# Kernel tuning notes

Measured on AMD Instinct MI355X. Metric: run time of the kernel, lower is better.

The kernel has to match this reference:

```python
import jax, jax.numpy as jnp
import numpy as np
import math

B, NTOK, NH, D = 8, 1000, 8, 64
CHUNK = 8  # query-chunk size for the pairwise L1 score computation


def _linearm(w, x):
    # LinearM: w [out, in+1] (last column is bias); x [b, t, in] -> [b, t, out]
    return jnp.einsum('oi,bti->bto', w[:, :-1], x) + w[:, -1]


def setup_inputs() -> dict:
    key = jax.random.key(0)
    ks = jax.random.split(key, 4)
    scl = 0.005
    x = jax.random.normal(ks[0], (B, NTOK, D), dtype=jnp.float32)
    wq = (scl * jax.random.normal(ks[1], (NH * D, D + 1), dtype=jnp.float32)).at[:, -1].set(0.0)
    wv = (scl * jax.random.normal(ks[2], (NH * D, D + 1), dtype=jnp.float32)).at[:, -1].set(0.0)
    wk = scl * jnp.ones((NH, D), dtype=jnp.float32)
    wf = (scl * jax.random.normal(ks[3], (D, D + 1), dtype=jnp.float32)).at[:, -1].set(0.0)
    return {"x": x, "wq": wq, "wv": wv, "wk": wk, "wf": wf}


def _forward(x, wq, wv, wk, wf):
    b, t, d = x.shape
    nh = wk.shape[0]
    scale = 1.0 / math.sqrt(d)

    q = _linearm(wq, x).reshape(b, t, nh, d)          # [b, t, nh, d]
    v = _linearm(wv, x).reshape(b, t, nh, d)          # [b, t, nh, d]
    k = x[:, :, None, :] * wk[None, None]             # [b, t, nh, d]

    # L1-distance attention scores: a[b, s, q, h] = -scale * sum_w |q[b,q,h,w] - k[b,s,h,w]|
    # Computed in query chunks so the [b, t, t, nh, d] pairwise tensor is never materialized.
    nc = t // CHUNK
    qc = q.reshape(b, nc, CHUNK, nh, d).transpose(1, 0, 2, 3, 4)  # [nc, b, C, nh, d]

    @jax.checkpoint
    def scores(qch):
        # qch: [b, C, nh, d] -> [b, t(src), C, nh]
        return -scale * jnp.sum(jnp.abs(qch[:, None] - k[:, :, None]), axis=-1)

    a = jax.lax.map(scores, qc)                       # [nc, b, t, C, nh]
    a = a.transpose(1, 2, 0, 3, 4).reshape(b, t, t, nh)  # [b, src, dst, nh]

    # Extra all-zero "null" source row (mirrors a[:, a2len, :, :] = 0 before softmax)
    a = jnp.concatenate([a, jnp.zeros((b, 1, t, nh), a.dtype)], axis=1)
    a = jax.nn.softmax(a, axis=1)[:, :t]              # softmax over sources, drop null row

    # einsum('bsdh,bshw->bdhw') followed by sum over heads, fused:
    out = jnp.einsum('bsth,bshw->btw', a, v)          # [b, t, d]

    y = jax.nn.relu(out)                              # self.gelu is actually ReLU
    y = _linearm(wf, y)
    return x + y


def reference(x, wq, wv, wk, wf):
    return _forward(x, wq, wv, wk, wf)
```

## Files before the change

### kernel.cpp

```cpp
#include <hip/hip_runtime.h>
#include <math.h>

#define Bb 8
#define Tt 1000
#define TPAD 1024
#define NHh 8
#define Dd 64

typedef short bf16x8 __attribute__((ext_vector_type(8)));
typedef float f32x4 __attribute__((ext_vector_type(4)));

#define QOFF (-0.3f)
#define QSTEP (0.6f / 256.0f)
#define QINV (256.0f / 0.6f)
#define CQ (-0.125f * 1.44269504088896341f * QSTEP)

__device__ __forceinline__ unsigned sad_u8(unsigned a, unsigned b, unsigned c) {
#if __has_builtin(__builtin_amdgcn_sad_u8)
    return __builtin_amdgcn_sad_u8(a, b, c);
#else
    unsigned d;
    asm("v_sad_u8 %0, %1, %2, %3" : "=v"(d) : "v"(a), "v"(b), "v"(c));
    return d;
#endif
}

__device__ __forceinline__ unsigned quant8(float v) {
    float t = (v - QOFF) * QINV + 0.5f;
    t = fminf(fmaxf(t, 0.0f), 255.0f);
    return (unsigned)(int)t;
}

__device__ __forceinline__ unsigned cvt_pk_bf16(float lo, float hi) {
    unsigned r;
    asm("v_cvt_pk_bf16_f32 %0, %1, %2" : "=v"(r) : "v"(lo), "v"(hi));
    return r;
}

__device__ __forceinline__ bf16x8 mkbf(unsigned u0, unsigned u1, unsigned u2, unsigned u3) {
    union { unsigned u[4]; bf16x8 v; } x;
    x.u[0] = u0; x.u[1] = u1; x.u[2] = u2; x.u[3] = u3;
    return x.v;
}

__device__ __forceinline__ bf16x8 bfc(uint4 q) {
    union { uint4 q; bf16x8 v; } x; x.q = q; return x.v;
}

#define GLDS(gsrc, ldst) \
    __builtin_amdgcn_global_load_lds((const __attribute__((address_space(1))) unsigned*)(gsrc), \
                                     (__attribute__((address_space(3))) unsigned*)(ldst), 16, 0, 0)

__global__ __launch_bounds__(256) void prep_kernel(
    const float* __restrict__ x, const float* __restrict__ wq,
    const float* __restrict__ wv, const float* __restrict__ wk,
    unsigned* __restrict__ qq8, unsigned* __restrict__ kq8,
    uint4* __restrict__ vfrag)
{
    __shared__ float xs[64][68];
    __shared__ float ws[64][65];
    __shared__ float vS[64][68];
    const int tid = threadIdx.x;
    const int st = blockIdx.x;
    const int cb = blockIdx.y;
    const int b  = blockIdx.z;
    const bool isQ = (cb < 8);
    const int h = isQ ? cb : (cb - 8);
    const float* W = isQ ? wq : wv;
    const int cBase = h * 64;
    const int bh = b * NHh + h;

#pragma unroll
    for (int i = 0; i < 4; ++i) {
        int f4 = tid + i * 256;
        int r = f4 >> 4, c4 = (f4 & 15) << 2;
        int row = st * 64 + r; if (row >= Tt) row = Tt - 1;
        *(float4*)&xs[r][c4] = *(const float4*)&x[((size_t)b * Tt + row) * 64 + c4];
    }
#pragma unroll
    for (int i = 0; i < 16; ++i) {
        int idx = tid + i * 256;
        int c = idx >> 6, k = idx & 63;
        ws[c][k] = W[(cBase + c) * 65 + k];
    }
    __syncthreads();

    const int rg = tid >> 4, cg = tid & 15;
    const int r0 = rg * 4, c0 = cg * 4;
    float acc[4][4];
#pragma unroll
    for (int j = 0; j < 4; ++j) {
        float bias = W[(cBase + c0 + j) * 65 + 64];
#pragma unroll
        for (int i = 0; i < 4; ++i) acc[i][j] = bias;
    }
    for (int k0 = 0; k0 < 64; k0 += 4) {
        float4 a[4];
#pragma unroll
        for (int i = 0; i < 4; ++i) a[i] = *(const float4*)&xs[r0 + i][k0];
#pragma unroll
        for (int j = 0; j < 4; ++j) {
            float b0 = ws[c0 + j][k0 + 0];
            float b1 = ws[c0 + j][k0 + 1];
            float b2 = ws[c0 + j][k0 + 2];
            float b3 = ws[c0 + j][k0 + 3];
#pragma unroll
            for (int i = 0; i < 4; ++i)
                acc[i][j] += a[i].x * b0 + a[i].y * b1 + a[i].z * b2 + a[i].w * b3;
        }
    }

    if (isQ) {
#pragma unroll
        for (int i = 0; i < 4; ++i) {
            int t = st * 64 + r0 + i;
            unsigned d = 0u;
            if (t < Tt)
                d = quant8(acc[i][0]) | (quant8(acc[i][1]) << 8) |
                    (quant8(acc[i][2]) << 16) | (quant8(acc[i][3]) << 24);
            qq8[((size_t)bh * TPAD + t) * 16 + cg] = d;
        }
        {
            const int r = tid >> 2, c4 = tid & 3;
            const int t = st * 64 + r;
            unsigned kd[4];
            if (t < Tt) {
#pragma unroll
                for (int dw = 0; dw < 4; ++dw) {
                    int w = c4 * 16 + dw * 4;
                    float4 wkv = *(const float4*)&wk[h * 64 + w];
                    kd[dw] = quant8(xs[r][w + 0] * wkv.x) |
                             (quant8(xs[r][w + 1] * wkv.y) << 8) |
                             (quant8(xs[r][w + 2] * wkv.z) << 16) |
                             (quant8(xs[r][w + 3] * wkv.w) << 24);
                }
            } else {
                kd[0] = kd[1] = kd[2] = kd[3] = 0u;
            }
            const int c4s = c4 ^ ((r >> 3) & 3);
            *(uint4*)&kq8[((size_t)bh * TPAD + t) * 16 + c4s * 4] =
                make_uint4(kd[0], kd[1], kd[2], kd[3]);
        }
    } else {
#pragma unroll
        for (int i = 0; i < 4; ++i) {
            float4 o; o.x = acc[i][0]; o.y = acc[i][1]; o.z = acc[i][2]; o.w = acc[i][3];
            *(float4*)&vS[r0 + i][c0] = o;
        }
        __syncthreads();
#pragma unroll
        for (int e2 = 0; e2 < 2; ++e2) {
            int ent = tid + e2 * 256;
            int kk = ent >> 8, rem = ent & 255, n = rem >> 6, lane = rem & 63;
            int ts = kk * 32 + ((lane >> 4) << 3);
            int w  = n * 16 + (lane & 15);
            unsigned o[4];
#pragma unroll
            for (int pr = 0; pr < 4; ++pr) {
                int t0 = st * 64 + ts + pr * 2;
                float lo = (t0 < Tt)     ? vS[ts + pr * 2][w]     : 0.0f;
                float hi = (t0 + 1 < Tt) ? vS[ts + pr * 2 + 1][w] : 0.0f;
                o[pr] = cvt_pk_bf16(lo, hi);
            }
            vfrag[(((size_t)bh * 16 + st) * 8 + (kk * 4 + n)) * 64 + lane] =
                make_uint4(o[0], o[1], o[2], o[3]);
        }
    }
}

__global__ __launch_bounds__(256) void attn_kernel(
    const unsigned* __restrict__ qq8, const unsigned* __restrict__ kq8,
    const uint4* __restrict__ vfrag, float* __restrict__ part)
{
    __shared__ uint4 smem[1024];
    __shared__ float dred[2][2][16];

    const int tid = threadIdx.x;
    const int wv_ = tid >> 6;
    const int l   = tid & 63;
    const int g   = l >> 4;
    const int m   = l & 15;
    const int qt  = blockIdx.x;
    const int h   = blockIdx.y, b = blockIdx.z;
    const int bh  = b * NHh + h;
    const int rowhalf  = wv_ & 1;
    const int tilehalf = wv_ >> 1;
    const int rowbase  = qt * 64 + rowhalf * 32;

    unsigned qa[16], qb[16];
    {
        const uint4* qp = (const uint4*)qq8 + ((size_t)bh * TPAD + rowbase + m) * 4;
        *(uint4*)&qa[0]  = qp[0];  *(uint4*)&qa[4]  = qp[1];
        *(uint4*)&qa[8]  = qp[2];  *(uint4*)&qa[12] = qp[3];
        const uint4* qp2 = qp + 64;
        *(uint4*)&qb[0]  = qp2[0]; *(uint4*)&qb[4]  = qp2[1];
        *(uint4*)&qb[8]  = qp2[2]; *(uint4*)&qb[12] = qp2[3];
    }

    const uint4* kg = (const uint4*)kq8 + (size_t)bh * 4096;
    const uint4* vg = vfrag + (size_t)bh * 8192;

#define STAGEK(I, BUF) do { \
        GLDS(kg + (I) * 256 + wv_ * 64 + l,       &smem[(0 * 2 + (BUF)) * 256 + wv_ * 64]); \
        GLDS(kg + (8 + (I)) * 256 + wv_ * 64 + l, &smem[(1 * 2 + (BUF)) * 256 + wv_ * 64]); \
    } while (0)

    STAGEK(0, 0);
    __syncthreads();

    f32x4 aca[4], acb[4];
#pragma unroll
    for (int n = 0; n < 4; ++n) { aca[n] = (f32x4){0.f,0.f,0.f,0.f}; acb[n] = aca[n]; }
    float dsum_a = 0.0f, dsum_b = 0.0f;

#pragma unroll 1
    for (int i = 0; i < 8; ++i) {
        const int cur = i & 1;
        const int t = tilehalf * 8 + i;
        const uint4* kbase = &smem[(tilehalf * 2 + cur) * 256];
        const uint4* vt = vg + (size_t)t * 512 + l;

        if (i < 7) STAGEK(i + 1, cur ^ 1);

        uint4 vf0 = vt[0 * 64], vf1 = vt[1 * 64], vf2 = vt[2 * 64], vf3 = vt[3 * 64];

        bf16x8 Aa0, Ab0;
        {
            float pa[8], pb[8];
#pragma unroll
            for (int e = 0; e < 8; ++e) {
                const uint4* kb = kbase + ((g << 3) + e) * 4;
                uint4 c0 = kb[0 ^ g], c1 = kb[1 ^ g], c2 = kb[2 ^ g], c3 = kb[3 ^ g];
                const unsigned* k0 = (const unsigned*)&c0;
                const unsigned* k1 = (const unsigned*)&c1;
                const unsigned* k2 = (const unsigned*)&c2;
                const unsigned* k3 = (const unsigned*)&c3;
                unsigned sa0 = 0u, sa1 = 0u, sb0 = 0u, sb1 = 0u;
#pragma unroll
                for (int w = 0; w < 4; ++w) {
                    sa0 = sad_u8(qa[w],      k0[w], sa0);
                    sa1 = sad_u8(qa[4 + w],  k1[w], sa1);
                    sb0 = sad_u8(qb[w],      k0[w], sb0);
                    sb1 = sad_u8(qb[4 + w],  k1[w], sb1);
                }
#pragma unroll
                for (int w = 0; w < 4; ++w) {
                    sa0 = sad_u8(qa[8 + w],  k2[w], sa0);
                    sa1 = sad_u8(qa[12 + w], k3[w], sa1);
                    sb0 = sad_u8(qb[8 + w],  k2[w], sb0);
                    sb1 = sad_u8(qb[12 + w], k3[w], sb1);
                }
                pa[e] = __builtin_amdgcn_exp2f(CQ * (float)(sa0 + sa1));
                pb[e] = __builtin_amdgcn_exp2f(CQ * (float)(sb0 + sb1));
                dsum_a += pa[e];
                dsum_b += pb[e];
            }
            Aa0 = mkbf(cvt_pk_bf16(pa[0], pa[1]), cvt_pk_bf16(pa[2], pa[3]),
                       cvt_pk_bf16(pa[4], pa[5]), cvt_pk_bf16(pa[6], pa[7]));
            Ab0 = mkbf(cvt_pk_bf16(pb[0], pb[1]), cvt_pk_bf16(pb[2], pb[3]),
                       cvt_pk_bf16(pb[4], pb[5]), cvt_pk_bf16(pb[6], pb[7]));
        }

        aca[0] = __builtin_amdgcn_mfma_f32_16x16x32_bf16(Aa0, bfc(vf0), aca[0], 0, 0, 0);
        acb[0] = __builtin_amdgcn_mfma_f32_16x16x32_bf16(Ab0, bfc(vf0), acb[0], 0, 0, 0);
        aca[1] = __builtin_amdgcn_mfma_f32_16x16x32_bf16(Aa0, bfc(vf1), aca[1], 0, 0, 0);
        acb[1] = __builtin_amdgcn_mfma_f32_16x16x32_bf16(Ab0, bfc(vf1), acb[1], 0, 0, 0);
        aca[2] = __builtin_amdgcn_mfma_f32_16x16x32_bf16(Aa0, bfc(vf2), aca[2], 0, 0, 0);
        acb[2] = __builtin_amdgcn_mfma_f32_16x16x32_bf16(Ab0, bfc(vf2), acb[2], 0, 0, 0);
        aca[3] = __builtin_amdgcn_mfma_f32_16x16x32_bf16(Aa0, bfc(vf3), aca[3], 0, 0, 0);
        acb[3] = __builtin_amdgcn_mfma_f32_16x16x32_bf16(Ab0, bfc(vf3), acb[3], 0, 0, 0);

        uint4 vf4 = vt[4 * 64], vf5 = vt[5 * 64], vf6 = vt[6 * 64], vf7 = vt[7 * 64];

        bf16x8 Aa1, Ab1;
        {
            const bool maskall = (t == 15) && (g >= 1);
            float pa[8], pb[8];
#pragma unroll
            for (int e = 0; e < 8; ++e) {
                const uint4* kb = kbase + (32 + (g << 3) + e) * 4;
                uint4 c0 = kb[0 ^ g], c1 = kb[1 ^ g], c2 = kb[2 ^ g], c3 = kb[3 ^ g];
                const unsigned* k0 = (const unsigned*)&c0;
                const unsigned* k1 = (const unsigned*)&c1;
                const unsigned* k2 = (const unsigned*)&c2;
                const unsigned* k3 = (const unsigned*)&c3;
                unsigned sa0 = 0u, sa1 = 0u, sb0 = 0u, sb1 = 0u;
#pragma unroll
                for (int w = 0; w < 4; ++w) {
                    sa0 = sad_u8(qa[w],      k0[w], sa0);
                    sa1 = sad_u8(qa[4 + w],  k1[w], sa1);
                    sb0 = sad_u8(qb[w],      k0[w], sb0);
                    sb1 = sad_u8(qb[4 + w],  k1[w], sb1);
                }
#pragma unroll
                for (int w = 0; w < 4; ++w) {
                    sa0 = sad_u8(qa[8 + w],  k2[w], sa0);
                    sa1 = sad_u8(qa[12 + w], k3[w], sa1);
                    sb0 = sad_u8(qb[8 + w],  k2[w], sb0);
                    sb1 = sad_u8(qb[12 + w], k3[w], sb1);
                }
                pa[e] = maskall ? 0.0f : __builtin_amdgcn_exp2f(CQ * (float)(sa0 + sa1));
                pb[e] = maskall ? 0.0f : __builtin_amdgcn_exp2f(CQ * (float)(sb0 + sb1));
                dsum_a += pa[e];
                dsum_b += pb[e];
            }
            Aa1 = mkbf(cvt_pk_bf16(pa[0], pa[1]), cvt_pk_bf16(pa[2], pa[3]),
                       cvt_pk_bf16(pa[4], pa[5]), cvt_pk_bf16(pa[6], pa[7]));
            Ab1 = mkbf(cvt_pk_bf16(pb[0], pb[1]), cvt_pk_bf16(pb[2], pb[3]),
                       cvt_pk_bf16(pb[4], pb[5]), cvt_pk_bf16(pb[6], pb[7]));
        }

        aca[0] = __builtin_amdgcn_mfma_f32_16x16x32_bf16(Aa1, bfc(vf4), aca[0], 0, 0, 0);
        acb[0] = __builtin_amdgcn_mfma_f32_16x16x32_bf16(Ab1, bfc(vf4), acb[0], 0, 0, 0);
        aca[1] = __builtin_amdgcn_mfma_f32_16x16x32_bf16(Aa1, bfc(vf5), aca[1], 0, 0, 0);
        acb[1] = __builtin_amdgcn_mfma_f32_16x16x32_bf16(Ab1, bfc(vf5), acb[1], 0, 0, 0);
        aca[2] = __builtin_amdgcn_mfma_f32_16x16x32_bf16(Aa1, bfc(vf6), aca[2], 0, 0, 0);
        acb[2] = __builtin_amdgcn_mfma_f32_16x16x32_bf16(Ab1, bfc(vf6), acb[2], 0, 0, 0);
        aca[3] = __builtin_amdgcn_mfma_f32_16x16x32_bf16(Aa1, bfc(vf7), aca[3], 0, 0, 0);
        acb[3] = __builtin_amdgcn_mfma_f32_16x16x32_bf16(Ab1, bfc(vf7), acb[3], 0, 0, 0);

        __syncthreads();
    }
#undef STAGEK

    dsum_a += __shfl_xor(dsum_a, 16);
    dsum_a += __shfl_xor(dsum_a, 32);
    dsum_b += __shfl_xor(dsum_b, 16);
    dsum_b += __shfl_xor(dsum_b, 32);

    f32x4* red = (f32x4*)smem;
    if (tilehalf == 1) {
#pragma unroll
        for (int n = 0; n < 4; ++n) {
            red[(((rowhalf * 2 + 0) * 4) + n) * 64 + l] = aca[n];
            red[(((rowhalf * 2 + 1) * 4) + n) * 64 + l] = acb[n];
        }
        if (l < 16) { dred[rowhalf][0][l] = dsum_a; dred[rowhalf][1][l] = dsum_b; }
    }
    __syncthreads();
    if (tilehalf == 0) {
#pragma unroll
        for (int n = 0; n < 4; ++n) {
            f32x4 ra = red[(((rowhalf * 2 + 0) * 4) + n) * 64 + l];
            f32x4 rb = red[(((rowhalf * 2 + 1) * 4) + n) * 64 + l];
#pragma unroll
            for (int j = 0; j < 4; ++j) { aca[n][j] += ra[j]; acb[n][j] += rb[j]; }
        }
        const float den_a = 1.0f + dsum_a + dred[rowhalf][0][m];
        const float den_b = 1.0f + dsum_b + dred[rowhalf][1][m];

#pragma unroll
        for (int j = 0; j < 4; ++j) {
            float dja = __shfl(den_a, g * 4 + j);
            float djb = __shfl(den_b, g * 4 + j);
            int row_a = rowbase + g * 4 + j;
            int row_b = rowbase + 16 + g * 4 + j;
            if (row_a < Tt) {
                float inv = 1.0f / dja;
                float* o = part + (((size_t)b * Tt + row_a) * NHh + h) * 64 + m;
                o[0]  = aca[0][j] * inv;
                o[16] = aca[1][j] * inv;
                o[32] = aca[2][j] * inv;
                o[48] = aca[3][j] * inv;
            }
            if (row_b < Tt) {
                float inv = 1.0f / djb;
                float* o = part + (((size_t)b * Tt + row_b) * NHh + h) * 64 + m;
                o[0]  = acb[0][j] * inv;
                o[16] = acb[1][j] * inv;
                o[32] = acb[2][j] * inv;
                o[48] = acb[3][j] * inv;
            }
        }
    }
}

__global__ __launch_bounds__(256) void finalize_kernel(
    const float* __restrict__ x, const float* __restrict__ wf,
    const float* __restrict__ part, float* __restrict__ out)
{
    __shared__ float wfs[64][65];
    __shared__ float osh[4][64];
    const int tid = threadIdx.x;
    for (int i = tid; i < 64 * 65; i += 256) wfs[i / 65][i % 65] = wf[i];
    const int wave = tid >> 6, lane = tid & 63;
    const int token = blockIdx.x * 4 + wave;
    float o = 0.f;
    const float* pt = part + (size_t)token * NHh * Dd;
#pragma unroll
    for (int hh = 0; hh < NHh; ++hh) o += pt[hh * Dd + lane];
    o = fmaxf(o, 0.f);
    osh[wave][lane] = o;
    __syncthreads();
    float acc = wfs[lane][64];
#pragma unroll 8
    for (int w = 0; w < 64; ++w) acc += wfs[lane][w] * osh[wave][w];
    out[(size_t)token * Dd + lane] = x[(size_t)token * Dd + lane] + acc;
}

extern "C" void kernel_launch(void* const* d_in, const int* in_sizes, int n_in,
                              void* d_out, int out_size, void* d_ws, size_t ws_size,
                              hipStream_t stream)
{
    const float* x  = (const float*)d_in[0];
    const float* wq = (const float*)d_in[1];
    const float* wv = (const float*)d_in[2];
    const float* wk = (const float*)d_in[3];
    const float* wf = (const float*)d_in[4];
    float* out = (float*)d_out;

    char* base = (char*)d_ws;
    float*    part  = (float*)base;
    unsigned* qq8   = (unsigned*)(base + 16384000);
    unsigned* kq8   = (unsigned*)(base + 16384000 + 4194304);
    uint4*    vfrag = (uint4*)(base + 16384000 + 2 * 4194304);

    prep_kernel<<<dim3(16, 16, Bb), 256, 0, stream>>>(x, wq, wv, wk, qq8, kq8, vfrag);
    attn_kernel<<<dim3(16, NHh, Bb), 256, 0, stream>>>(qq8, kq8, vfrag, part);
    finalize_kernel<<<2000, 256, 0, stream>>>(x, wf, part, out);
}
```

Before: 92.25 us.

## Split attention source dimension across two blocks and combine partials in finalize

The attention grid doubles along z so each block handles half of the source tiles, 4 per wave pair instead of 8. Unnormalized numerators are written as bf16 partials and the denominator partial sums are written separately. The finalize kernel now combines the two halves and divides by the softmax denominator there. This raises parallelism from 1024 to 2048 blocks to fill the GPU better, at the cost of extra partial-result traffic and bf16 rounding of the numerators.

```diff
diff --git a/kernel.cpp b/kernel.cpp
--- a/kernel.cpp
+++ b/kernel.cpp
@@ -35,6 +35,14 @@
     unsigned r;
     asm("v_cvt_pk_bf16_f32 %0, %1, %2" : "=v"(r) : "v"(lo), "v"(hi));
     return r;
+}
+
+__device__ __forceinline__ unsigned short f2bf(float v) {
+    return (unsigned short)(cvt_pk_bf16(v, v) & 0xffffu);
+}
+
+__device__ __forceinline__ float bf2f(unsigned short u) {
+    union { unsigned u; float f; } x; x.u = ((unsigned)u) << 16; return x.f;
 }
 
 __device__ __forceinline__ bf16x8 mkbf(unsigned u0, unsigned u1, unsigned u2, unsigned u3) {
@@ -170,7 +178,8 @@
 
 __global__ __launch_bounds__(256) void attn_kernel(
     const unsigned* __restrict__ qq8, const unsigned* __restrict__ kq8,
-    const uint4* __restrict__ vfrag, float* __restrict__ part)
+    const uint4* __restrict__ vfrag,
+    unsigned short* __restrict__ numbf, float* __restrict__ dsums)
 {
     __shared__ uint4 smem[1024];
     __shared__ float dred[2][2][16];
@@ -181,11 +190,15 @@
     const int g   = l >> 4;
     const int m   = l & 15;
     const int qt  = blockIdx.x;
-    const int h   = blockIdx.y, b = blockIdx.z;
+    const int h   = blockIdx.y;
+    const int bz  = blockIdx.z;
+    const int b   = bz >> 1;
+    const int half = bz & 1;
     const int bh  = b * NHh + h;
-    const int rowhalf  = wv_ & 1;
-    const int tilehalf = wv_ >> 1;
-    const int rowbase  = qt * 64 + rowhalf * 32;
+    const int rowhalf = wv_ & 1;
+    const int tileq   = wv_ >> 1;
+    const int rowbase = qt * 64 + rowhalf * 32;
+    const int tbase   = half * 8 + tileq * 4;
 
     unsigned qa[16], qb[16];
     {
@@ -201,8 +214,8 @@
     const uint4* vg = vfrag + (size_t)bh * 8192;
 
 #define STAGEK(I, BUF) do { \
-        GLDS(kg + (I) * 256 + wv_ * 64 + l,       &smem[(0 * 2 + (BUF)) * 256 + wv_ * 64]); \
-        GLDS(kg + (8 + (I)) * 256 + wv_ * 64 + l, &smem[(1 * 2 + (BUF)) * 256 + wv_ * 64]); \
+        GLDS(kg + (half * 8 + (I)) * 256 + wv_ * 64 + l,     &smem[(0 * 2 + (BUF)) * 256 + wv_ * 64]); \
+        GLDS(kg + (half * 8 + 4 + (I)) * 256 + wv_ * 64 + l, &smem[(1 * 2 + (BUF)) * 256 + wv_ * 64]); \
     } while (0)
 
     STAGEK(0, 0);
@@ -214,19 +227,20 @@
     float dsum_a = 0.0f, dsum_b = 0.0f;
 
 #pragma unroll 1
-    for (int i = 0; i < 8; ++i) {
+    for (int i = 0; i < 4; ++i) {
         const int cur = i & 1;
-        const int t = tilehalf * 8 + i;
-        const uint4* kbase = &smem[(tilehalf * 2 + cur) * 256];
+        const int t = tbase + i;
+        const uint4* kbase = &smem[(tileq * 2 + cur) * 256];
         const uint4* vt = vg + (size_t)t * 512 + l;
 
-        if (i < 7) STAGEK(i + 1, cur ^ 1);
+        if (i < 3) STAGEK(i + 1, cur ^ 1);
 
         uint4 vf0 = vt[0 * 64], vf1 = vt[1 * 64], vf2 = vt[2 * 64], vf3 = vt[3 * 64];
 
         bf16x8 Aa0, Ab0;
         {
-            float pa[8], pb[8];
+            unsigned wa[4], wb[4];
+            float pva = 0.f, pvb = 0.f;
 #pragma unroll
             for (int e = 0; e < 8; ++e) {
                 const uint4* kb = kbase + ((g << 3) + e) * 4;
@@ -250,15 +264,14 @@
                     sb0 = sad_u8(qb[8 + w],  k2[w], sb0);
                     sb1 = sad_u8(qb[12 + w], k3[w], sb1);
                 }
-                pa[e] = __builtin_amdgcn_exp2f(CQ * (float)(sa0 + sa1));
-                pb[e] = __builtin_amdgcn_exp2f(CQ * (float)(sb0 + sb1));
-                dsum_a += pa[e];
-                dsum_b += pb[e];
-            }
-            Aa0 = mkbf(cvt_pk_bf16(pa[0], pa[1]), cvt_pk_bf16(pa[2], pa[3]),
-                       cvt_pk_bf16(pa[4], pa[5]), cvt_pk_bf16(pa[6], pa[7]));
-            Ab0 = mkbf(cvt_pk_bf16(pb[0], pb[1]), cvt_pk_bf16(pb[2], pb[3]),
-                       cvt_pk_bf16(pb[4], pb[5]), cvt_pk_bf16(pb[6], pb[7]));
+                float pea = __builtin_amdgcn_exp2f(CQ * (float)(sa0 + sa1));
+                float peb = __builtin_amdgcn_exp2f(CQ * (float)(sb0 + sb1));
+                dsum_a += pea; dsum_b += peb;
+                if (e & 1) { wa[e >> 1] = cvt_pk_bf16(pva, pea); wb[e >> 1] = cvt_pk_bf16(pvb, peb); }
+                else       { pva = pea; pvb = peb; }
+            }
+            Aa0 = mkbf(wa[0], wa[1], wa[2], wa[3]);
+            Ab0 = mkbf(wb[0], wb[1], wb[2], wb[3]);
         }
 
         aca[0] = __builtin_amdgcn_mfma_f32_16x16x32_bf16(Aa0, bfc(vf0), aca[0], 0, 0, 0);
@@ -275,7 +288,8 @@
         bf16x8 Aa1, Ab1;
         {
             const bool maskall = (t == 15) && (g >= 1);
-            float pa[8], pb[8];
+            unsigned wa[4], wb[4];
+            float pva = 0.f, pvb = 0.f;
 #pragma unroll
             for (int e = 0; e < 8; ++e) {
                 const uint4* kb = kbase + (32 + (g << 3) + e) * 4;
@@ -299,15 +313,14 @@
                     sb0 = sad_u8(qb[8 + w],  k2[w], sb0);
                     sb1 = sad_u8(qb[12 + w], k3[w], sb1);
                 }
-                pa[e] = maskall ? 0.0f : __builtin_amdgcn_exp2f(CQ * (float)(sa0 + sa1));
-                pb[e] = maskall ? 0.0f : __builtin_amdgcn_exp2f(CQ * (float)(sb0 + sb1));
-                dsum_a += pa[e];
-                dsum_b += pb[e];
-            }
-            Aa1 = mkbf(cvt_pk_bf16(pa[0], pa[1]), cvt_pk_bf16(pa[2], pa[3]),
-                       cvt_pk_bf16(pa[4], pa[5]), cvt_pk_bf16(pa[6], pa[7]));
-            Ab1 = mkbf(cvt_pk_bf16(pb[0], pb[1]), cvt_pk_bf16(pb[2], pb[3]),
-                       cvt_pk_bf16(pb[4], pb[5]), cvt_pk_bf16(pb[6], pb[7]));
+                float pea = maskall ? 0.0f : __builtin_amdgcn_exp2f(CQ * (float)(sa0 + sa1));
+                float peb = maskall ? 0.0f : __builtin_amdgcn_exp2f(CQ * (float)(sb0 + sb1));
+                dsum_a += pea; dsum_b += peb;
+                if (e & 1) { wa[e >> 1] = cvt_pk_bf16(pva, pea); wb[e >> 1] = cvt_pk_bf16(pvb, peb); }
+                else       { pva = pea; pvb = peb; }
+            }
+            Aa1 = mkbf(wa[0], wa[1], wa[2], wa[3]);
+            Ab1 = mkbf(wb[0], wb[1], wb[2], wb[3]);
         }
 
         aca[0] = __builtin_amdgcn_mfma_f32_16x16x32_bf16(Aa1, bfc(vf4), aca[0], 0, 0, 0);
@@ -329,7 +342,7 @@
     dsum_b += __shfl_xor(dsum_b, 32);
 
     f32x4* red = (f32x4*)smem;
-    if (tilehalf == 1) {
+    if (tileq == 1) {
 #pragma unroll
         for (int n = 0; n < 4; ++n) {
             red[(((rowhalf * 2 + 0) * 4) + n) * 64 + l] = aca[n];
@@ -338,7 +351,7 @@
         if (l < 16) { dred[rowhalf][0][l] = dsum_a; dred[rowhalf][1][l] = dsum_b; }
     }
     __syncthreads();
-    if (tilehalf == 0) {
+    if (tileq == 0) {
 #pragma unroll
         for (int n = 0; n < 4; ++n) {
             f32x4 ra = red[(((rowhalf * 2 + 0) * 4) + n) * 64 + l];
@@ -346,38 +359,40 @@
 #pragma unroll
             for (int j = 0; j < 4; ++j) { aca[n][j] += ra[j]; acb[n][j] += rb[j]; }
         }
-        const float den_a = 1.0f + dsum_a + dred[rowhalf][0][m];
-        const float den_b = 1.0f + dsum_b + dred[rowhalf][1][m];
+        const float dta = dsum_a + dred[rowhalf][0][m];
+        const float dtb = dsum_b + dred[rowhalf][1][m];
 
 #pragma unroll
         for (int j = 0; j < 4; ++j) {
-            float dja = __shfl(den_a, g * 4 + j);
-            float djb = __shfl(den_b, g * 4 + j);
             int row_a = rowbase + g * 4 + j;
             int row_b = rowbase + 16 + g * 4 + j;
             if (row_a < Tt) {
-                float inv = 1.0f / dja;
-                float* o = part + (((size_t)b * Tt + row_a) * NHh + h) * 64 + m;
-                o[0]  = aca[0][j] * inv;
-                o[16] = aca[1][j] * inv;
-                o[32] = aca[2][j] * inv;
-                o[48] = aca[3][j] * inv;
+                unsigned short* o = numbf + (((size_t)(b * Tt + row_a) * 16) + h * 2 + half) * 64 + m;
+                o[0]  = f2bf(aca[0][j]);
+                o[16] = f2bf(aca[1][j]);
+                o[32] = f2bf(aca[2][j]);
+                o[48] = f2bf(aca[3][j]);
             }
             if (row_b < Tt) {
-                float inv = 1.0f / djb;
-                float* o = part + (((size_t)b * Tt + row_b) * NHh + h) * 64 + m;
-                o[0]  = acb[0][j] * inv;
-                o[16] = acb[1][j] * inv;
-                o[32] = acb[2][j] * inv;
-                o[48] = acb[3][j] * inv;
-            }
+                unsigned short* o = numbf + (((size_t)(b * Tt + row_b) * 16) + h * 2 + half) * 64 + m;
+                o[0]  = f2bf(acb[0][j]);
+                o[16] = f2bf(acb[1][j]);
+                o[32] = f2bf(acb[2][j]);
+                o[48] = f2bf(acb[3][j]);
+            }
+        }
+        if (l < 16) {
+            int ra = rowbase + m, rb = rowbase + 16 + m;
+            if (ra < Tt) dsums[(((size_t)(b * Tt + ra) * 8) + h) * 2 + half] = dta;
+            if (rb < Tt) dsums[(((size_t)(b * Tt + rb) * 8) + h) * 2 + half] = dtb;
         }
     }
 }
 
 __global__ __launch_bounds__(256) void finalize_kernel(
     const float* __restrict__ x, const float* __restrict__ wf,
-    const float* __restrict__ part, float* __restrict__ out)
+    const unsigned short* __restrict__ numbf, const float* __restrict__ dsums,
+    float* __restrict__ out)
 {
     __shared__ float wfs[64][65];
     __shared__ float osh[4][64];
@@ -385,10 +400,18 @@
     for (int i = tid; i < 64 * 65; i += 256) wfs[i / 65][i % 65] = wf[i];
     const int wave = tid >> 6, lane = tid & 63;
     const int token = blockIdx.x * 4 + wave;
+
+    const float dsv = dsums[(size_t)token * 16 + (lane & 15)];
+    const unsigned short* np = numbf + (size_t)token * 1024;
     float o = 0.f;
-    const float* pt = part + (size_t)token * NHh * Dd;
-#pragma unroll
-    for (int hh = 0; hh < NHh; ++hh) o += pt[hh * Dd + lane];
+#pragma unroll
+    for (int hh = 0; hh < 8; ++hh) {
+        float den = 1.0f + __shfl(dsv, 2 * hh) + __shfl(dsv, 2 * hh + 1);
+        float inv = 1.0f / den;
+        float a0 = bf2f(np[(2 * hh) * 64 + lane]);
+        float a1 = bf2f(np[(2 * hh + 1) * 64 + lane]);
+        o += (a0 + a1) * inv;
+    }
     o = fmaxf(o, 0.f);
     osh[wave][lane] = o;
     __syncthreads();
@@ -410,12 +433,13 @@
     float* out = (float*)d_out;
 
     char* base = (char*)d_ws;
-    float*    part  = (float*)base;
-    unsigned* qq8   = (unsigned*)(base + 16384000);
-    unsigned* kq8   = (unsigned*)(base + 16384000 + 4194304);
-    uint4*    vfrag = (uint4*)(base + 16384000 + 2 * 4194304);
+    unsigned short* numbf = (unsigned short*)base;
+    float*    dsums = (float*)(base + 16384000);
+    unsigned* qq8   = (unsigned*)(base + 16896000);
+    unsigned* kq8   = (unsigned*)(base + 16896000 + 4194304);
+    uint4*    vfrag = (uint4*)(base + 16896000 + 2 * 4194304);
 
     prep_kernel<<<dim3(16, 16, Bb), 256, 0, stream>>>(x, wq, wv, wk, qq8, kq8, vfrag);
-    attn_kernel<<<dim3(16, NHh, Bb), 256, 0, stream>>>(qq8, kq8, vfrag, part);
-    finalize_kernel<<<2000, 256, 0, stream>>>(x, wf, part, out);
-}
+    attn_kernel<<<dim3(16, NHh, 2 * Bb), 256, 0, stream>>>(qq8, kq8, vfrag, numbf, dsums);
+    finalize_kernel<<<2000, 256, 0, stream>>>(x, wf, numbf, dsums, out);
+}
```

New measurement: 92.00 us. Within noise of the previous version (-0.3%).
